# Kernel optimization log

Hardware: AMD Instinct MI355X
Metric: run time of the kernel (lower is better)

Reference implementation:

```python
import jax, jax.numpy as jnp
import numpy as np

DIMS = 1024
FF_DIMS = 4096
EPS = 1e-5


def _ln(x, g, b):
    m = jnp.mean(x, axis=-1, keepdims=True)
    v = jnp.mean(jnp.square(x - m), axis=-1, keepdims=True)
    return (x - m) * jax.lax.rsqrt(v + EPS) * g + b


def _bind(a, b):
    # HRR bind = circular convolution via FFT
    n = b.shape[-1]
    return jnp.fft.irfft(jnp.fft.rfft(a) * jnp.fft.rfft(b), n=n)


def _unbind(s, a):
    # HRR unbind = circular correlation (bind with approximate inverse) = conj in freq
    n = s.shape[-1]
    return jnp.fft.irfft(jnp.fft.rfft(s) * jnp.conj(jnp.fft.rfft(a)), n=n)


def setup_inputs() -> dict:
    key = jax.random.key(0)
    ks = jax.random.split(key, 16)
    d, f = DIMS, FF_DIMS
    s_d = 1.0 / np.sqrt(d)
    s_f = 1.0 / np.sqrt(f)
    return {
        "x": jax.random.normal(ks[0], (4, 4096, d), jnp.float32),
        "Wq": jax.random.normal(ks[1], (d, d), jnp.float32) * s_d,
        "bq": jnp.zeros((d,), jnp.float32),
        "gq": jnp.ones((d,), jnp.float32),
        "betaq": jnp.zeros((d,), jnp.float32),
        "Wk": jax.random.normal(ks[2], (d, d), jnp.float32) * s_d,
        "bk": jnp.zeros((d,), jnp.float32),
        "gk": jnp.ones((d,), jnp.float32),
        "betak": jnp.zeros((d,), jnp.float32),
        "g0": jnp.ones((d,), jnp.float32),
        "beta0": jnp.zeros((d,), jnp.float32),
        "W1": jax.random.normal(ks[3], (f, d), jnp.float32) * s_d,
        "b1": jnp.zeros((f,), jnp.float32),
        "W2": jax.random.normal(ks[4], (d, f), jnp.float32) * s_f,
        "b2": jnp.zeros((d,), jnp.float32),
        "g1": jnp.ones((d,), jnp.float32),
        "beta1": jnp.zeros((d,), jnp.float32),
    }


def reference(x, Wq, bq, gq, betaq, Wk, bk, gk, betak, g0, beta0,
              W1, b1, W2, b2, g1, beta1):
    # HolographicMixer (dropout is identity in eval)
    q = _ln(jnp.einsum('bse,de->bsd', x, Wq) + bq, gq, betaq)
    k = _ln(jnp.einsum('bse,de->bsd', x, Wk) + bk, gk, betak)
    xb = _bind(k, x)                      # (B,S,D)
    s = jnp.sum(xb, axis=1, keepdims=True)  # (B,1,D)
    vals = _unbind(s, q)                  # broadcast (B,1,D)x(B,S,D)->(B,S,D)
    mix = xb + vals
    x = _ln(x + mix, g0, beta0)
    # FeedForward
    h = jax.nn.relu(jnp.einsum('bsd,fd->bsf', x, W1) + b1)
    ff = jnp.einsum('bsf,df->bsd', h, W2) + b2
    x = _ln(x + ff, g1, beta1)
    return x
```

## Files before the change

### kernel.cpp

```cpp
#include <hip/hip_runtime.h>

typedef unsigned short u16;
typedef unsigned int   u32;
typedef __attribute__((ext_vector_type(8))) __bf16 bf16x8;
typedef __attribute__((ext_vector_type(4))) float   f32x4;

#define NT   16384
#define DD   1024
#define FFD  4096

#define SREG  ((size_t)33554432)
#define S1O   ((size_t)0)
#define S2O   (SREG)
#define S3O   (2*SREG)
#define S4O   (3*SREG)
#define O_WQ  (4*SREG)
#define O_WK  (O_WQ + (size_t)2097152)
#define O_W1  (O_WK + (size_t)2097152)
#define O_W2  (O_W1 + (size_t)8388608)
#define O_FWD (O_W2 + (size_t)8388608)
#define O_INV (O_FWD + (size_t)2097152)
#define O_SF  (O_INV + (size_t)2097152)

__device__ __forceinline__ float b2f(u16 h) {
    u32 u = ((u32)h) << 16;
    return __uint_as_float(u);
}
__device__ __forceinline__ u16 f2b(float f) {
    u32 u = __float_as_uint(f);
    u32 r = (u + 0x7FFFu + ((u >> 16) & 1u)) >> 16;
    return (u16)r;
}

__device__ __forceinline__ void ld16(const u16* g, u16* l) {
    __builtin_amdgcn_global_load_lds(
        (const __attribute__((address_space(1))) void*)g,
        (__attribute__((address_space(3))) void*)l, 16, 0, 0);
}

__device__ __forceinline__ void block_red2(float& a, float& b, float* red, int tid) {
#pragma unroll
    for (int off = 32; off; off >>= 1) {
        a += __shfl_down(a, off, 64);
        b += __shfl_down(b, off, 64);
    }
    int w = tid >> 6;
    if ((tid & 63) == 0) { red[w] = a; red[4 + w] = b; }
    __syncthreads();
    a = red[0] + red[1] + red[2] + red[3];
    b = red[4] + red[5] + red[6] + red[7];
}

__global__ void zero_sf_k(float* __restrict__ Sf) {
    int i = blockIdx.x * 256 + threadIdx.x;
    if (i < 4096) Sf[i] = 0.f;
}

__global__ void cast_f32_bf16_k(const float* __restrict__ s, u16* __restrict__ d, int n4) {
    int i = blockIdx.x * 256 + threadIdx.x;
    if (i < n4) {
        float4 v = ((const float4*)s)[i];
        ushort4 o;
        o.x = f2b(v.x); o.y = f2b(v.y); o.z = f2b(v.z); o.w = f2b(v.w);
        ((ushort4*)d)[i] = o;
    }
}

__global__ void gen_fwd_k(u16* __restrict__ Fwd) {
    int idx = blockIdx.x * 256 + threadIdx.x;
    int n = idx >> 10, k = idx & 1023;
    int f  = (n == 0) ? 0 : ((n & 1) ? ((n + 1) >> 1) : (n >> 1));
    bool re = (n == 0) || (n & 1);
    int r = (f * k) & 1023;
    float ang = (float)r * 6.1359233e-3f;
    float v = re ? __cosf(ang) : -__sinf(ang);
    Fwd[idx] = f2b(v);
}
__global__ void gen_inv_k(u16* __restrict__ Inv) {
    int idx = blockIdx.x * 256 + threadIdx.x;
    int d = idx >> 10, n = idx & 1023;
    int f  = (n == 0) ? 0 : ((n & 1) ? ((n + 1) >> 1) : (n >> 1));
    bool re = (n == 0) || (n & 1);
    int r = (f * d) & 1023;
    float ang = (float)r * 6.1359233e-3f;
    float c = (f == 0 || f == 512) ? (1.0f / 1024.0f) : (2.0f / 1024.0f);
    float v = re ? c * __cosf(ang) : -c * __sinf(ang);
    Inv[idx] = f2b(v);
}

#define BM 128
#define BN 128
#define BK 64
#define EPI_BF16            0
#define EPI_BIAS_BF16       1
#define EPI_BIAS_RELU_BF16  2
#define EPI_BIAS_ADDB_F32   3
#define EPI_ADD_F32         4

template <int EPI>
__global__ __launch_bounds__(256, 3) void gemm_bt_k(
    const u16* __restrict__ A, const u16* __restrict__ B, void* __restrict__ Cout,
    const float* __restrict__ bias, const u16* __restrict__ addp16,
    int K, int lda, int ldb, int ldc)
{
    __shared__ __align__(16) u16 As[BM * BK];
    __shared__ __align__(16) u16 Bs[BN * BK];
    const int tid = threadIdx.x;

    int m0, n0;
    {
        const int id = blockIdx.y * gridDim.x + blockIdx.x;
        const int nb = gridDim.x * gridDim.y;
        if ((nb & 7) == 0) {
            const int per = nb >> 3;
            const int t = (id & 7) * per + (id >> 3);
            n0 = (t % gridDim.x) * BN;
            m0 = (t / gridDim.x) * BM;
        } else {
            n0 = blockIdx.x * BN;
            m0 = blockIdx.y * BM;
        }
    }

    const int w = tid >> 6, l = tid & 63;
    const int wm = (w >> 1) << 6, wn = (w & 1) << 6;
    const int tm = l & 15, quad = l >> 4;
    const int sw = (tm & 7) << 3;

    f32x4 acc[4][4] = {};

    const int sr = tid >> 3;
    const int sc = ((tid & 7) ^ (sr & 7)) << 3;
    const u16* Ag = A + (size_t)(m0 + sr) * lda;
    const u16* Bg = B + (size_t)(n0 + sr) * ldb;
    u16* Asl = As + tid * 8;
    u16* Bsl = Bs + tid * 8;
    const size_t a32 = (size_t)32 * lda, b32 = (size_t)32 * ldb;

    for (int k0 = 0; k0 < K; k0 += BK) {
#pragma unroll
        for (int i = 0; i < 4; ++i) {
            ld16(Ag + (size_t)i * a32 + k0 + sc, Asl + i * 2048);
            ld16(Bg + (size_t)i * b32 + k0 + sc, Bsl + i * 2048);
        }
        __syncthreads();
#pragma unroll
        for (int kk = 0; kk < BK; kk += 32) {
            bf16x8 af[4], bfr[4];
#pragma unroll
            for (int i = 0; i < 4; ++i)
                af[i] = *(const bf16x8*)(const void*)(As + (wm + i * 16 + tm) * BK + ((((kk >> 3) + quad) << 3) ^ sw));
#pragma unroll
            for (int j = 0; j < 4; ++j)
                bfr[j] = *(const bf16x8*)(const void*)(Bs + (wn + j * 16 + tm) * BK + ((((kk >> 3) + quad) << 3) ^ sw));
#pragma unroll
            for (int i = 0; i < 4; ++i)
#pragma unroll
                for (int j = 0; j < 4; ++j)
                    acc[i][j] = __builtin_amdgcn_mfma_f32_16x16x32_bf16(af[i], bfr[j], acc[i][j], 0, 0, 0);
        }
        __syncthreads();
    }

#pragma unroll
    for (int i = 0; i < 4; ++i) {
        const int gmb = m0 + wm + i * 16 + quad * 4;
#pragma unroll
        for (int j = 0; j < 4; ++j) {
            const int gn = n0 + wn + j * 16 + tm;
            float bv = 0.f;
            if (EPI == EPI_BIAS_BF16 || EPI == EPI_BIAS_RELU_BF16 || EPI == EPI_BIAS_ADDB_F32)
                bv = bias[gn];
#pragma unroll
            for (int r = 0; r < 4; ++r) {
                size_t off = (size_t)(gmb + r) * ldc + gn;
                float v = acc[i][j][r] + bv;
                if (EPI == EPI_BIAS_ADDB_F32) v += b2f(addp16[off]);
                if (EPI == EPI_ADD_F32)       v += ((const float*)Cout)[off];
                if (EPI == EPI_BIAS_RELU_BF16) v = fmaxf(v, 0.f);
                if (EPI == EPI_BF16 || EPI == EPI_BIAS_BF16 || EPI == EPI_BIAS_RELU_BF16)
                    ((u16*)Cout)[off] = f2b(v);
                else
                    ((float*)Cout)[off] = v;
            }
        }
    }
}

__global__ void ln_bf16_k(const u16* __restrict__ src, u16* __restrict__ dst,
                          const float* __restrict__ g, const float* __restrict__ be) {
    __shared__ float red[8];
    const int t = blockIdx.x, tid = threadIdx.x;
    ushort4 h = ((const ushort4*)(src + (size_t)t * DD))[tid];
    float4 v = { b2f(h.x), b2f(h.y), b2f(h.z), b2f(h.w) };
    float s  = v.x + v.y + v.z + v.w;
    float ss = v.x * v.x + v.y * v.y + v.z * v.z + v.w * v.w;
    block_red2(s, ss, red, tid);
    float mean = s * (1.f / 1024.f);
    float inv  = 1.0f / sqrtf(ss * (1.f / 1024.f) - mean * mean + 1e-5f);
    float4 gv = ((const float4*)g)[tid];
    float4 bv = ((const float4*)be)[tid];
    ushort4 o;
    o.x = f2b((v.x - mean) * inv * gv.x + bv.x);
    o.y = f2b((v.y - mean) * inv * gv.y + bv.y);
    o.z = f2b((v.z - mean) * inv * gv.z + bv.z);
    o.w = f2b((v.w - mean) * inv * gv.w + bv.w);
    ((ushort4*)(dst + (size_t)t * DD))[tid] = o;
}

__global__ void ln_out_k(float* __restrict__ io, const float* __restrict__ g,
                         const float* __restrict__ be) {
    __shared__ float red[8];
    const int t = blockIdx.x, tid = threadIdx.x;
    float4 v = ((const float4*)(io + (size_t)t * DD))[tid];
    float s  = v.x + v.y + v.z + v.w;
    float ss = v.x * v.x + v.y * v.y + v.z * v.z + v.w * v.w;
    block_red2(s, ss, red, tid);
    float mean = s * (1.f / 1024.f);
    float inv  = 1.0f / sqrtf(ss * (1.f / 1024.f) - mean * mean + 1e-5f);
    float4 gv = ((const float4*)g)[tid];
    float4 bv = ((const float4*)be)[tid];
    float4 o;
    o.x = (v.x - mean) * inv * gv.x + bv.x;
    o.y = (v.y - mean) * inv * gv.y + bv.y;
    o.z = (v.z - mean) * inv * gv.z + bv.z;
    o.w = (v.w - mean) * inv * gv.w + bv.w;
    ((float4*)(io + (size_t)t * DD))[tid] = o;
}

#define PW1_TOK 16
__global__ void pw1_k(const u16* __restrict__ FTx, const u16* __restrict__ FTk,
                      float* __restrict__ Sf) {
    const int tid = threadIdx.x;
    const int t0 = blockIdx.x * PW1_TOK;
    const int b = t0 >> 12;
    float a0 = 0.f;
    float ar1 = 0.f, ai1 = 0.f;
    float ar2 = 0.f, ai2 = 0.f;
    const int f1 = tid + 1, f2 = tid + 257;
    for (int it = 0; it < PW1_TOK; ++it) {
        const size_t ro = (size_t)(t0 + it) * DD;
        const u16* rx = FTx + ro;
        const u16* rk = FTk + ro;
        if (tid == 0) a0 += b2f(rk[0]) * b2f(rx[0]);
        {
            float xr = b2f(rx[2 * f1 - 1]), xi = b2f(rx[2 * f1]);
            float kr = b2f(rk[2 * f1 - 1]), ki = b2f(rk[2 * f1]);
            ar1 += kr * xr - ki * xi;
            ai1 += kr * xi + ki * xr;
        }
        if (f2 < 512) {
            float xr = b2f(rx[2 * f2 - 1]), xi = b2f(rx[2 * f2]);
            float kr = b2f(rk[2 * f2 - 1]), ki = b2f(rk[2 * f2]);
            ar2 += kr * xr - ki * xi;
            ai2 += kr * xi + ki * xr;
        } else {
            ar2 += b2f(rk[1023]) * b2f(rx[1023]);
        }
    }
    float* sb = Sf + (size_t)b * DD;
    if (tid == 0) atomicAdd(&sb[0], a0);
    atomicAdd(&sb[2 * f1 - 1], ar1);
    atomicAdd(&sb[2 * f1],     ai1);
    if (f2 < 512) {
        atomicAdd(&sb[2 * f2 - 1], ar2);
        atomicAdd(&sb[2 * f2],     ai2);
    } else {
        atomicAdd(&sb[1023], ar2);
    }
}

__global__ void pw2_k(u16* __restrict__ FTx, const u16* __restrict__ FTk,
                      const u16* __restrict__ FTq, const float* __restrict__ Sf) {
    const int t = blockIdx.x, tid = threadIdx.x;
    const int b = t >> 12;
    const size_t ro = (size_t)t * DD;
    u16* rx = FTx + ro;
    const u16* rk = FTk + ro;
    const u16* rq = FTq + ro;
    const float* sb = Sf + (size_t)b * DD;
    const int f1 = tid + 1, f2 = tid + 257;
    if (tid == 0) {
        float x = b2f(rx[0]), k = b2f(rk[0]), q = b2f(rq[0]);
        rx[0] = f2b(x + k * x + sb[0] * q);
    }
    {
        float xr = b2f(rx[2 * f1 - 1]), xi = b2f(rx[2 * f1]);
        float kr = b2f(rk[2 * f1 - 1]), ki = b2f(rk[2 * f1]);
        float qr = b2f(rq[2 * f1 - 1]), qi = b2f(rq[2 * f1]);
        float sr = sb[2 * f1 - 1], si = sb[2 * f1];
        rx[2 * f1 - 1] = f2b(xr + (kr * xr - ki * xi) + (sr * qr + si * qi));
        rx[2 * f1]     = f2b(xi + (kr * xi + ki * xr) + (si * qr - sr * qi));
    }
    if (f2 < 512) {
        float xr = b2f(rx[2 * f2 - 1]), xi = b2f(rx[2 * f2]);
        float kr = b2f(rk[2 * f2 - 1]), ki = b2f(rk[2 * f2]);
        float qr = b2f(rq[2 * f2 - 1]), qi = b2f(rq[2 * f2]);
        float sr = sb[2 * f2 - 1], si = sb[2 * f2];
        rx[2 * f2 - 1] = f2b(xr + (kr * xr - ki * xi) + (sr * qr + si * qi));
        rx[2 * f2]     = f2b(xi + (kr * xi + ki * xr) + (si * qr - sr * qi));
    } else {
        float x = b2f(rx[1023]), k = b2f(rk[1023]), q = b2f(rq[1023]);
        rx[1023] = f2b(x + k * x + sb[1023] * q);
    }
}

extern "C" void kernel_launch(void* const* d_in, const int* in_sizes, int n_in,
                              void* d_out, int out_size, void* d_ws, size_t ws_size,
                              hipStream_t stream) {
    const float* x     = (const float*)d_in[0];
    const float* Wq    = (const float*)d_in[1];
    const float* bq    = (const float*)d_in[2];
    const float* gq    = (const float*)d_in[3];
    const float* betaq = (const float*)d_in[4];
    const float* Wk    = (const float*)d_in[5];
    const float* bk    = (const float*)d_in[6];
    const float* gk    = (const float*)d_in[7];
    const float* betak = (const float*)d_in[8];
    const float* g0    = (const float*)d_in[9];
    const float* beta0 = (const float*)d_in[10];
    const float* W1    = (const float*)d_in[11];
    const float* b1    = (const float*)d_in[12];
    const float* W2    = (const float*)d_in[13];
    const float* b2    = (const float*)d_in[14];
    const float* g1    = (const float*)d_in[15];
    const float* beta1 = (const float*)d_in[16];

    char* ws = (char*)d_ws;
    u16* S1 = (u16*)(ws + S1O);
    u16* S2 = (u16*)(ws + S2O);
    u16* S3 = (u16*)(ws + S3O);
    u16* S4 = (u16*)(ws + S4O);
    u16* wq16 = (u16*)(ws + O_WQ);
    u16* wk16 = (u16*)(ws + O_WK);
    u16* w116 = (u16*)(ws + O_W1);
    u16* w216 = (u16*)(ws + O_W2);
    u16* fwdP = (u16*)(ws + O_FWD);
    u16* invP = (u16*)(ws + O_INV);
    float* Sf = (float*)(ws + O_SF);
    float* out = (float*)d_out;

    zero_sf_k<<<16, 256, 0, stream>>>(Sf);
    cast_f32_bf16_k<<<16384, 256, 0, stream>>>(x, S1, 4194304);
    cast_f32_bf16_k<<<1024, 256, 0, stream>>>(Wq, wq16, 262144);
    cast_f32_bf16_k<<<1024, 256, 0, stream>>>(Wk, wk16, 262144);
    cast_f32_bf16_k<<<4096, 256, 0, stream>>>(W1, w116, 1048576);
    cast_f32_bf16_k<<<4096, 256, 0, stream>>>(W2, w216, 1048576);
    gen_fwd_k<<<4096, 256, 0, stream>>>(fwdP);
    gen_inv_k<<<4096, 256, 0, stream>>>(invP);

    gemm_bt_k<EPI_BIAS_BF16><<<dim3(8, 128), 256, 0, stream>>>(S1, wq16, S2, bq, nullptr, 1024, 1024, 1024, 1024);
    gemm_bt_k<EPI_BIAS_BF16><<<dim3(8, 128), 256, 0, stream>>>(S1, wk16, S3, bk, nullptr, 1024, 1024, 1024, 1024);
    ln_bf16_k<<<NT, 256, 0, stream>>>(S2, S2, gq, betaq);
    ln_bf16_k<<<NT, 256, 0, stream>>>(S3, S3, gk, betak);

    gemm_bt_k<EPI_BF16><<<dim3(8, 128), 256, 0, stream>>>(S1, fwdP, S4, nullptr, nullptr, 1024, 1024, 1024, 1024);
    gemm_bt_k<EPI_BF16><<<dim3(8, 128), 256, 0, stream>>>(S3, fwdP, S1, nullptr, nullptr, 1024, 1024, 1024, 1024);
    gemm_bt_k<EPI_BF16><<<dim3(8, 128), 256, 0, stream>>>(S2, fwdP, S3, nullptr, nullptr, 1024, 1024, 1024, 1024);

    pw1_k<<<NT / PW1_TOK, 256, 0, stream>>>(S4, S1, Sf);
    pw2_k<<<NT, 256, 0, stream>>>(S4, S1, S3, Sf);

    gemm_bt_k<EPI_BF16><<<dim3(8, 128), 256, 0, stream>>>(S4, invP, S2, nullptr, nullptr, 1024, 1024, 1024, 1024);

    ln_bf16_k<<<NT, 256, 0, stream>>>(S2, S1, g0, beta0);

    gemm_bt_k<EPI_BIAS_RELU_BF16><<<dim3(16, 128), 256, 0, stream>>>(S1, w116, S3, b1, nullptr, 1024, 1024, 1024, 2048);
    gemm_bt_k<EPI_BIAS_ADDB_F32><<<dim3(8, 128), 256, 0, stream>>>(S3, w216, out, b2, S1, 2048, 2048, 4096, 1024);
    gemm_bt_k<EPI_BIAS_RELU_BF16><<<dim3(16, 128), 256, 0, stream>>>(S1, w116 + (size_t)2048 * 1024, S3, b1 + 2048, nullptr, 1024, 1024, 1024, 2048);
    gemm_bt_k<EPI_ADD_F32><<<dim3(8, 128), 256, 0, stream>>>(S3, w216 + 2048, out, nullptr, nullptr, 2048, 2048, 4096, 1024);

    ln_out_k<<<NT, 256, 0, stream>>>(out, g1, beta1);

    (void)in_sizes; (void)n_in; (void)out_size; (void)ws_size;
}
```

Measured before the change: 786.8 us.

## Rewrite GEMM as 256x256 tile, 8-wave kernel with interleaved load/MFMA phases

Enlarges the GEMM tile from 128x128 to 256x256 and moves to 512 threads (8 waves, each owning a 128x64 sub-tile). The K loop is split into four quadrant phases that overlap the next tile's global-to-LDS loads with MFMA work on the current one, using explicit barriers, waitcnts and s_setprio. The goal is more data reuse per LDS byte and hiding of memory latency. In exchange the grids are smaller (256-512 blocks), so wave quantization on the CUs gets coarser. The single shared LDS buffer is overwritten in place, which relies on the exact barrier ordering for correctness.

```diff
diff --git a/kernel.cpp b/kernel.cpp
--- a/kernel.cpp
+++ b/kernel.cpp
@@ -88,8 +88,8 @@
     Inv[idx] = f2b(v);
 }
 
-#define BM 128
-#define BN 128
+#define BM 256
+#define BN 256
 #define BK 64
 #define EPI_BF16            0
 #define EPI_BIAS_BF16       1
@@ -97,8 +97,13 @@
 #define EPI_BIAS_ADDB_F32   3
 #define EPI_ADD_F32         4
 
+#define MFMA16 __builtin_amdgcn_mfma_f32_16x16x32_bf16
+#define BARRIER()    asm volatile("s_barrier" ::: "memory")
+#define WAIT_LGKM0() asm volatile("s_waitcnt lgkmcnt(0)" ::: "memory")
+#define WAIT_VM0()   asm volatile("s_waitcnt vmcnt(0)" ::: "memory")
+
 template <int EPI>
-__global__ __launch_bounds__(256, 3) void gemm_bt_k(
+__global__ __launch_bounds__(512, 2) void gemm_bt_k(
     const u16* __restrict__ A, const u16* __restrict__ B, void* __restrict__ Cout,
     const float* __restrict__ bias, const u16* __restrict__ addp16,
     int K, int lda, int ldb, int ldc)
@@ -122,49 +127,119 @@
         }
     }
 
-    const int w = tid >> 6, l = tid & 63;
-    const int wm = (w >> 1) << 6, wn = (w & 1) << 6;
+    const int wid = tid >> 6, l = tid & 63;
+    const int wm = (wid >> 2) << 7;
+    const int wn = (wid & 3) << 6;
     const int tm = l & 15, quad = l >> 4;
-    const int sw = (tm & 7) << 3;
-
-    f32x4 acc[4][4] = {};
-
-    const int sr = tid >> 3;
-    const int sc = ((tid & 7) ^ (sr & 7)) << 3;
-    const u16* Ag = A + (size_t)(m0 + sr) * lda;
-    const u16* Bg = B + (size_t)(n0 + sr) * ldb;
+    const int cx0 = ((quad ^ (tm & 7)) << 3);
+    const int cx1 = (((quad + 4) ^ (tm & 7)) << 3);
+
+    f32x4 acc[8][4] = {};
+
+    const int srow = tid >> 3;
+    const int scol = ((tid & 7) ^ (srow & 7)) << 3;
+    const u16* Ag = A + (size_t)(m0 + srow) * lda + scol;
+    const u16* Bg = B + (size_t)(n0 + srow) * ldb + scol;
     u16* Asl = As + tid * 8;
     u16* Bsl = Bs + tid * 8;
-    const size_t a32 = (size_t)32 * lda, b32 = (size_t)32 * ldb;
-
-    for (int k0 = 0; k0 < K; k0 += BK) {
+    const size_t a64 = (size_t)64 * lda, b64 = (size_t)64 * ldb;
+
+    const u16* ArA = As + (wm + tm) * BK;
+    const u16* ArB = Bs + (wn + tm) * BK;
+
+    const int ntk = K >> 6;
+
+#pragma unroll
+    for (int h = 0; h < 4; ++h) {
+        ld16(Ag + (size_t)h * a64, Asl + h * 4096);
+        ld16(Bg + (size_t)h * b64, Bsl + h * 4096);
+    }
+    WAIT_VM0();
+    BARRIER();
+
+    for (int t = 0; t < ntk; ++t) {
+        const size_t kn = (size_t)(((t + 1 < ntk) ? (t + 1) : t) << 6);
+        bf16x8 a[4][2], bA[2][2], bB[2][2];
+
 #pragma unroll
         for (int i = 0; i < 4; ++i) {
-            ld16(Ag + (size_t)i * a32 + k0 + sc, Asl + i * 2048);
-            ld16(Bg + (size_t)i * b32 + k0 + sc, Bsl + i * 2048);
-        }
-        __syncthreads();
-#pragma unroll
-        for (int kk = 0; kk < BK; kk += 32) {
-            bf16x8 af[4], bfr[4];
-#pragma unroll
-            for (int i = 0; i < 4; ++i)
-                af[i] = *(const bf16x8*)(const void*)(As + (wm + i * 16 + tm) * BK + ((((kk >> 3) + quad) << 3) ^ sw));
-#pragma unroll
-            for (int j = 0; j < 4; ++j)
-                bfr[j] = *(const bf16x8*)(const void*)(Bs + (wn + j * 16 + tm) * BK + ((((kk >> 3) + quad) << 3) ^ sw));
-#pragma unroll
-            for (int i = 0; i < 4; ++i)
-#pragma unroll
-                for (int j = 0; j < 4; ++j)
-                    acc[i][j] = __builtin_amdgcn_mfma_f32_16x16x32_bf16(af[i], bfr[j], acc[i][j], 0, 0, 0);
-        }
-        __syncthreads();
-    }
-
-#pragma unroll
-    for (int i = 0; i < 4; ++i) {
-        const int gmb = m0 + wm + i * 16 + quad * 4;
+            a[i][0] = *(const bf16x8*)(const void*)(ArA + i * 1024 + cx0);
+            a[i][1] = *(const bf16x8*)(const void*)(ArA + i * 1024 + cx1);
+        }
+#pragma unroll
+        for (int j = 0; j < 2; ++j) {
+            bA[j][0] = *(const bf16x8*)(const void*)(ArB + j * 1024 + cx0);
+            bA[j][1] = *(const bf16x8*)(const void*)(ArB + j * 1024 + cx1);
+        }
+        WAIT_LGKM0();
+        __builtin_amdgcn_s_setprio(1);
+#pragma unroll
+        for (int i = 0; i < 4; ++i)
+#pragma unroll
+            for (int j = 0; j < 2; ++j) {
+                acc[i][j] = MFMA16(a[i][0], bA[j][0], acc[i][j], 0, 0, 0);
+                acc[i][j] = MFMA16(a[i][1], bA[j][1], acc[i][j], 0, 0, 0);
+            }
+        __builtin_amdgcn_s_setprio(0);
+        BARRIER();
+
+        ld16(Ag + kn,                 Asl);
+        ld16(Ag + kn + 2 * a64,       Asl + 2 * 4096);
+#pragma unroll
+        for (int j = 0; j < 2; ++j) {
+            bB[j][0] = *(const bf16x8*)(const void*)(ArB + (2 + j) * 1024 + cx0);
+            bB[j][1] = *(const bf16x8*)(const void*)(ArB + (2 + j) * 1024 + cx1);
+        }
+        WAIT_LGKM0();
+        __builtin_amdgcn_s_setprio(1);
+#pragma unroll
+        for (int i = 0; i < 4; ++i)
+#pragma unroll
+            for (int j = 0; j < 2; ++j) {
+                acc[i][2 + j] = MFMA16(a[i][0], bB[j][0], acc[i][2 + j], 0, 0, 0);
+                acc[i][2 + j] = MFMA16(a[i][1], bB[j][1], acc[i][2 + j], 0, 0, 0);
+            }
+        __builtin_amdgcn_s_setprio(0);
+        BARRIER();
+
+#pragma unroll
+        for (int h = 0; h < 4; ++h)
+            ld16(Bg + kn + (size_t)h * b64, Bsl + h * 4096);
+#pragma unroll
+        for (int i = 0; i < 4; ++i) {
+            a[i][0] = *(const bf16x8*)(const void*)(ArA + (4 + i) * 1024 + cx0);
+            a[i][1] = *(const bf16x8*)(const void*)(ArA + (4 + i) * 1024 + cx1);
+        }
+        WAIT_LGKM0();
+        __builtin_amdgcn_s_setprio(1);
+#pragma unroll
+        for (int i = 0; i < 4; ++i)
+#pragma unroll
+            for (int j = 0; j < 2; ++j) {
+                acc[4 + i][2 + j] = MFMA16(a[i][0], bB[j][0], acc[4 + i][2 + j], 0, 0, 0);
+                acc[4 + i][2 + j] = MFMA16(a[i][1], bB[j][1], acc[4 + i][2 + j], 0, 0, 0);
+            }
+        __builtin_amdgcn_s_setprio(0);
+        BARRIER();
+
+        ld16(Ag + kn + a64,           Asl + 4096);
+        ld16(Ag + kn + 3 * a64,       Asl + 3 * 4096);
+        __builtin_amdgcn_s_setprio(1);
+#pragma unroll
+        for (int i = 0; i < 4; ++i)
+#pragma unroll
+            for (int j = 0; j < 2; ++j) {
+                acc[4 + i][j] = MFMA16(a[i][0], bA[j][0], acc[4 + i][j], 0, 0, 0);
+                acc[4 + i][j] = MFMA16(a[i][1], bA[j][1], acc[4 + i][j], 0, 0, 0);
+            }
+        __builtin_amdgcn_s_setprio(0);
+        WAIT_VM0();
+        BARRIER();
+    }
+
+#pragma unroll
+    for (int i = 0; i < 8; ++i) {
+        const int gmb = m0 + wm + i * 16 + (quad << 2);
 #pragma unroll
         for (int j = 0; j < 4; ++j) {
             const int gn = n0 + wn + j * 16 + tm;
@@ -349,26 +424,26 @@
     gen_fwd_k<<<4096, 256, 0, stream>>>(fwdP);
     gen_inv_k<<<4096, 256, 0, stream>>>(invP);
 
-    gemm_bt_k<EPI_BIAS_BF16><<<dim3(8, 128), 256, 0, stream>>>(S1, wq16, S2, bq, nullptr, 1024, 1024, 1024, 1024);
-    gemm_bt_k<EPI_BIAS_BF16><<<dim3(8, 128), 256, 0, stream>>>(S1, wk16, S3, bk, nullptr, 1024, 1024, 1024, 1024);
+    gemm_bt_k<EPI_BIAS_BF16><<<dim3(4, 64), 512, 0, stream>>>(S1, wq16, S2, bq, nullptr, 1024, 1024, 1024, 1024);
+    gemm_bt_k<EPI_BIAS_BF16><<<dim3(4, 64), 512, 0, stream>>>(S1, wk16, S3, bk, nullptr, 1024, 1024, 1024, 1024);
     ln_bf16_k<<<NT, 256, 0, stream>>>(S2, S2, gq, betaq);
     ln_bf16_k<<<NT, 256, 0, stream>>>(S3, S3, gk, betak);
 
-    gemm_bt_k<EPI_BF16><<<dim3(8, 128), 256, 0, stream>>>(S1, fwdP, S4, nullptr, nullptr, 1024, 1024, 1024, 1024);
-    gemm_bt_k<EPI_BF16><<<dim3(8, 128), 256, 0, stream>>>(S3, fwdP, S1, nullptr, nullptr, 1024, 1024, 1024, 1024);
-    gemm_bt_k<EPI_BF16><<<dim3(8, 128), 256, 0, stream>>>(S2, fwdP, S3, nullptr, nullptr, 1024, 1024, 1024, 1024);
+    gemm_bt_k<EPI_BF16><<<dim3(4, 64), 512, 0, stream>>>(S1, fwdP, S4, nullptr, nullptr, 1024, 1024, 1024, 1024);
+    gemm_bt_k<EPI_BF16><<<dim3(4, 64), 512, 0, stream>>>(S3, fwdP, S1, nullptr, nullptr, 1024, 1024, 1024, 1024);
+    gemm_bt_k<EPI_BF16><<<dim3(4, 64), 512, 0, stream>>>(S2, fwdP, S3, nullptr, nullptr, 1024, 1024, 1024, 1024);
 
     pw1_k<<<NT / PW1_TOK, 256, 0, stream>>>(S4, S1, Sf);
     pw2_k<<<NT, 256, 0, stream>>>(S4, S1, S3, Sf);
 
-    gemm_bt_k<EPI_BF16><<<dim3(8, 128), 256, 0, stream>>>(S4, invP, S2, nullptr, nullptr, 1024, 1024, 1024, 1024);
+    gemm_bt_k<EPI_BF16><<<dim3(4, 64), 512, 0, stream>>>(S4, invP, S2, nullptr, nullptr, 1024, 1024, 1024, 1024);
 
     ln_bf16_k<<<NT, 256, 0, stream>>>(S2, S1, g0, beta0);
 
-    gemm_bt_k<EPI_BIAS_RELU_BF16><<<dim3(16, 128), 256, 0, stream>>>(S1, w116, S3, b1, nullptr, 1024, 1024, 1024, 2048);
-    gemm_bt_k<EPI_BIAS_ADDB_F32><<<dim3(8, 128), 256, 0, stream>>>(S3, w216, out, b2, S1, 2048, 2048, 4096, 1024);
-    gemm_bt_k<EPI_BIAS_RELU_BF16><<<dim3(16, 128), 256, 0, stream>>>(S1, w116 + (size_t)2048 * 1024, S3, b1 + 2048, nullptr, 1024, 1024, 1024, 2048);
-    gemm_bt_k<EPI_ADD_F32><<<dim3(8, 128), 256, 0, stream>>>(S3, w216 + 2048, out, nullptr, nullptr, 2048, 2048, 4096, 1024);
+    gemm_bt_k<EPI_BIAS_RELU_BF16><<<dim3(8, 64), 512, 0, stream>>>(S1, w116, S3, b1, nullptr, 1024, 1024, 1024, 2048);
+    gemm_bt_k<EPI_BIAS_ADDB_F32><<<dim3(4, 64), 512, 0, stream>>>(S3, w216, out, b2, S1, 2048, 2048, 4096, 1024);
+    gemm_bt_k<EPI_BIAS_RELU_BF16><<<dim3(8, 64), 512, 0, stream>>>(S1, w116 + (size_t)2048 * 1024, S3, b1 + 2048, nullptr, 1024, 1024, 1024, 2048);
+    gemm_bt_k<EPI_ADD_F32><<<dim3(4, 64), 512, 0, stream>>>(S3, w216 + 2048, out, nullptr, nullptr, 2048, 2048, 4096, 1024);
 
     ln_out_k<<<NT, 256, 0, stream>>>(out, g1, beta1);
 
```

New measurement: 878.6 us. 11.7% more time.

## Restructure GEMM to 256x256 tiles with double-buffered LDS prefetch pipeline

Applied to the files above, without the earlier changes.

The bf16 MFMA GEMM moves from 128x128 tiles with BK=64 and synchronous staging to 256x256 tiles with 512 threads and BK=32. LDS is double-buffered, and global-to-LDS loads for tile t+2 are issued while tile t is computed, using explicit vmcnt waits and raw barriers. Priority is raised around the MFMA block. The goals are more data reuse per block and hiding global load latency. The cost is higher register pressure (32 accumulators per thread) and fewer blocks (256 per GEMM), which may underfill 256 CUs.

```diff
diff --git a/kernel.cpp b/kernel.cpp
--- a/kernel.cpp
+++ b/kernel.cpp
@@ -88,23 +88,35 @@
     Inv[idx] = f2b(v);
 }
 
-#define BM 128
-#define BN 128
-#define BK 64
+#define BM 256
+#define BN 256
 #define EPI_BF16            0
 #define EPI_BIAS_BF16       1
 #define EPI_BIAS_RELU_BF16  2
 #define EPI_BIAS_ADDB_F32   3
 #define EPI_ADD_F32         4
 
+#define MFMA16 __builtin_amdgcn_mfma_f32_16x16x32_bf16
+#define BARRIER()    asm volatile("s_barrier" ::: "memory")
+#define WAIT_LGKM0() asm volatile("s_waitcnt lgkmcnt(0)" ::: "memory")
+#define WAIT_VM4()   asm volatile("s_waitcnt vmcnt(4)" ::: "memory")
+#define WAIT_VM0()   asm volatile("s_waitcnt vmcnt(0)" ::: "memory")
+
+#define STG(k0, b) do { \
+    ld16(Ag + (size_t)(k0),        Asl + (b) * 8192); \
+    ld16(Ag + (size_t)(k0) + a128, Asl + (b) * 8192 + 4096); \
+    ld16(Bg + (size_t)(k0),        Bsl + (b) * 8192); \
+    ld16(Bg + (size_t)(k0) + b128, Bsl + (b) * 8192 + 4096); \
+} while (0)
+
 template <int EPI>
-__global__ __launch_bounds__(256, 3) void gemm_bt_k(
+__global__ __launch_bounds__(512, 2) void gemm_bt_k(
     const u16* __restrict__ A, const u16* __restrict__ B, void* __restrict__ Cout,
     const float* __restrict__ bias, const u16* __restrict__ addp16,
     int K, int lda, int ldb, int ldc)
 {
-    __shared__ __align__(16) u16 As[BM * BK];
-    __shared__ __align__(16) u16 Bs[BN * BK];
+    __shared__ __align__(16) u16 As[2 * BM * 32];
+    __shared__ __align__(16) u16 Bs[2 * BN * 32];
     const int tid = threadIdx.x;
 
     int m0, n0;
@@ -122,49 +134,63 @@
         }
     }
 
-    const int w = tid >> 6, l = tid & 63;
-    const int wm = (w >> 1) << 6, wn = (w & 1) << 6;
+    const int wid = tid >> 6, l = tid & 63;
+    const int wm = (wid >> 2) << 7;
+    const int wn = (wid & 3) << 6;
     const int tm = l & 15, quad = l >> 4;
-    const int sw = (tm & 7) << 3;
-
-    f32x4 acc[4][4] = {};
-
-    const int sr = tid >> 3;
-    const int sc = ((tid & 7) ^ (sr & 7)) << 3;
-    const u16* Ag = A + (size_t)(m0 + sr) * lda;
-    const u16* Bg = B + (size_t)(n0 + sr) * ldb;
+    const int cx = (quad ^ ((tm >> 1) & 3)) << 3;
+
+    f32x4 acc[8][4] = {};
+
+    const int srow = tid >> 2;
+    const int scol = ((tid & 3) ^ ((tid >> 3) & 3)) << 3;
+    const u16* Ag = A + (size_t)(m0 + srow) * lda + scol;
+    const u16* Bg = B + (size_t)(n0 + srow) * ldb + scol;
     u16* Asl = As + tid * 8;
     u16* Bsl = Bs + tid * 8;
-    const size_t a32 = (size_t)32 * lda, b32 = (size_t)32 * ldb;
-
-    for (int k0 = 0; k0 < K; k0 += BK) {
-#pragma unroll
-        for (int i = 0; i < 4; ++i) {
-            ld16(Ag + (size_t)i * a32 + k0 + sc, Asl + i * 2048);
-            ld16(Bg + (size_t)i * b32 + k0 + sc, Bsl + i * 2048);
-        }
-        __syncthreads();
-#pragma unroll
-        for (int kk = 0; kk < BK; kk += 32) {
-            bf16x8 af[4], bfr[4];
-#pragma unroll
-            for (int i = 0; i < 4; ++i)
-                af[i] = *(const bf16x8*)(const void*)(As + (wm + i * 16 + tm) * BK + ((((kk >> 3) + quad) << 3) ^ sw));
+    const size_t a128 = (size_t)128 * lda, b128 = (size_t)128 * ldb;
+
+    const u16* Ard = As + (wm + tm) * 32 + cx;
+    const u16* Brd = Bs + (wn + tm) * 32 + cx;
+
+    const int ntk = K >> 5;
+
+    STG(0, 0);
+    STG(32, 1);
+    WAIT_VM4();
+    BARRIER();
+
+    for (int t = 0; t < ntk; ++t) {
+        const int buf = t & 1;
+        const int kf = ((t + 2 < ntk) ? (t + 2) : (ntk - 1)) << 5;
+        const u16* Ab = Ard + buf * 8192;
+        const u16* Bb = Brd + buf * 8192;
+
+        bf16x8 af[8], bfr[4];
+#pragma unroll
+        for (int i = 0; i < 8; ++i)
+            af[i] = *(const bf16x8*)(const void*)(Ab + i * 512);
+#pragma unroll
+        for (int j = 0; j < 4; ++j)
+            bfr[j] = *(const bf16x8*)(const void*)(Bb + j * 512);
+        WAIT_LGKM0();
+        BARRIER();
+        STG(kf, buf);
+        __builtin_amdgcn_s_setprio(1);
+#pragma unroll
+        for (int i = 0; i < 8; ++i)
 #pragma unroll
             for (int j = 0; j < 4; ++j)
-                bfr[j] = *(const bf16x8*)(const void*)(Bs + (wn + j * 16 + tm) * BK + ((((kk >> 3) + quad) << 3) ^ sw));
-#pragma unroll
-            for (int i = 0; i < 4; ++i)
-#pragma unroll
-                for (int j = 0; j < 4; ++j)
-                    acc[i][j] = __builtin_amdgcn_mfma_f32_16x16x32_bf16(af[i], bfr[j], acc[i][j], 0, 0, 0);
-        }
-        __syncthreads();
-    }
-
-#pragma unroll
-    for (int i = 0; i < 4; ++i) {
-        const int gmb = m0 + wm + i * 16 + quad * 4;
+                acc[i][j] = MFMA16(af[i], bfr[j], acc[i][j], 0, 0, 0);
+        __builtin_amdgcn_s_setprio(0);
+        WAIT_VM4();
+        BARRIER();
+    }
+    WAIT_VM0();
+
+#pragma unroll
+    for (int i = 0; i < 8; ++i) {
+        const int gmb = m0 + wm + i * 16 + (quad << 2);
 #pragma unroll
         for (int j = 0; j < 4; ++j) {
             const int gn = n0 + wn + j * 16 + tm;
@@ -349,26 +375,26 @@
     gen_fwd_k<<<4096, 256, 0, stream>>>(fwdP);
     gen_inv_k<<<4096, 256, 0, stream>>>(invP);
 
-    gemm_bt_k<EPI_BIAS_BF16><<<dim3(8, 128), 256, 0, stream>>>(S1, wq16, S2, bq, nullptr, 1024, 1024, 1024, 1024);
-    gemm_bt_k<EPI_BIAS_BF16><<<dim3(8, 128), 256, 0, stream>>>(S1, wk16, S3, bk, nullptr, 1024, 1024, 1024, 1024);
+    gemm_bt_k<EPI_BIAS_BF16><<<dim3(4, 64), 512, 0, stream>>>(S1, wq16, S2, bq, nullptr, 1024, 1024, 1024, 1024);
+    gemm_bt_k<EPI_BIAS_BF16><<<dim3(4, 64), 512, 0, stream>>>(S1, wk16, S3, bk, nullptr, 1024, 1024, 1024, 1024);
     ln_bf16_k<<<NT, 256, 0, stream>>>(S2, S2, gq, betaq);
     ln_bf16_k<<<NT, 256, 0, stream>>>(S3, S3, gk, betak);
 
-    gemm_bt_k<EPI_BF16><<<dim3(8, 128), 256, 0, stream>>>(S1, fwdP, S4, nullptr, nullptr, 1024, 1024, 1024, 1024);
-    gemm_bt_k<EPI_BF16><<<dim3(8, 128), 256, 0, stream>>>(S3, fwdP, S1, nullptr, nullptr, 1024, 1024, 1024, 1024);
-    gemm_bt_k<EPI_BF16><<<dim3(8, 128), 256, 0, stream>>>(S2, fwdP, S3, nullptr, nullptr, 1024, 1024, 1024, 1024);
+    gemm_bt_k<EPI_BF16><<<dim3(4, 64), 512, 0, stream>>>(S1, fwdP, S4, nullptr, nullptr, 1024, 1024, 1024, 1024);
+    gemm_bt_k<EPI_BF16><<<dim3(4, 64), 512, 0, stream>>>(S3, fwdP, S1, nullptr, nullptr, 1024, 1024, 1024, 1024);
+    gemm_bt_k<EPI_BF16><<<dim3(4, 64), 512, 0, stream>>>(S2, fwdP, S3, nullptr, nullptr, 1024, 1024, 1024, 1024);
 
     pw1_k<<<NT / PW1_TOK, 256, 0, stream>>>(S4, S1, Sf);
     pw2_k<<<NT, 256, 0, stream>>>(S4, S1, S3, Sf);
 
-    gemm_bt_k<EPI_BF16><<<dim3(8, 128), 256, 0, stream>>>(S4, invP, S2, nullptr, nullptr, 1024, 1024, 1024, 1024);
+    gemm_bt_k<EPI_BF16><<<dim3(4, 64), 512, 0, stream>>>(S4, invP, S2, nullptr, nullptr, 1024, 1024, 1024, 1024);
 
     ln_bf16_k<<<NT, 256, 0, stream>>>(S2, S1, g0, beta0);
 
-    gemm_bt_k<EPI_BIAS_RELU_BF16><<<dim3(16, 128), 256, 0, stream>>>(S1, w116, S3, b1, nullptr, 1024, 1024, 1024, 2048);
-    gemm_bt_k<EPI_BIAS_ADDB_F32><<<dim3(8, 128), 256, 0, stream>>>(S3, w216, out, b2, S1, 2048, 2048, 4096, 1024);
-    gemm_bt_k<EPI_BIAS_RELU_BF16><<<dim3(16, 128), 256, 0, stream>>>(S1, w116 + (size_t)2048 * 1024, S3, b1 + 2048, nullptr, 1024, 1024, 1024, 2048);
-    gemm_bt_k<EPI_ADD_F32><<<dim3(8, 128), 256, 0, stream>>>(S3, w216 + 2048, out, nullptr, nullptr, 2048, 2048, 4096, 1024);
+    gemm_bt_k<EPI_BIAS_RELU_BF16><<<dim3(8, 64), 512, 0, stream>>>(S1, w116, S3, b1, nullptr, 1024, 1024, 1024, 2048);
+    gemm_bt_k<EPI_BIAS_ADDB_F32><<<dim3(4, 64), 512, 0, stream>>>(S3, w216, out, b2, S1, 2048, 2048, 4096, 1024);
+    gemm_bt_k<EPI_BIAS_RELU_BF16><<<dim3(8, 64), 512, 0, stream>>>(S1, w116 + (size_t)2048 * 1024, S3, b1 + 2048, nullptr, 1024, 1024, 1024, 2048);
+    gemm_bt_k<EPI_ADD_F32><<<dim3(4, 64), 512, 0, stream>>>(S3, w216 + 2048, out, nullptr, nullptr, 2048, 2048, 4096, 1024);
 
     ln_out_k<<<NT, 256, 0, stream>>>(out, g1, beta1);
 
```

After: 843.1 us. 1.07x slower.
